# Kernel tuning notes

Measured on AMD Instinct MI355X. Metric: run time of the kernel, lower is better.

## Reference

```python
import jax, jax.numpy as jnp
import numpy as np

MODES = 12

def _conv3x3_circular(x, w, b):
    # x: [B,C,H,W], w: [O,I,3,3] -> circular padding of 1 then VALID conv
    xp = jnp.pad(x, ((0, 0), (0, 0), (1, 1), (1, 1)), mode='wrap')
    y = jax.lax.conv_general_dilated(xp, w, window_strides=(1, 1), padding='VALID',
                                     dimension_numbers=('NCHW', 'OIHW', 'NCHW'))
    return y + b[None, :, None, None]

def _spectral_conv(x, w1, w2):
    # x: [B,C,H,W] real; w1, w2: [C,O,m1,m2] complex
    B, C, H, W = x.shape
    x_ft = jnp.fft.rfft2(x)  # [B,C,H,W//2+1] complex
    m1 = min(MODES, H // 2)
    m2 = min(MODES, W // 2 + 1)
    top = jnp.einsum('bixy,ioxy->boxy', x_ft[:, :, :m1, :m2], w1[:, :, :m1, :m2])
    bot = jnp.einsum('bixy,ioxy->boxy', x_ft[:, :, -m1:, :m2], w2[:, :, :m1, :m2])
    out_ft = jnp.zeros((B, w1.shape[1], H, W // 2 + 1), dtype=x_ft.dtype)
    out_ft = out_ft.at[:, :, :m1, :m2].set(top).at[:, :, -m1:, :m2].set(bot)
    return jnp.fft.irfft2(out_ft, s=(H, W))

def setup_inputs() -> dict:
    key = jax.random.key(0)
    ks = jax.random.split(key, 16)
    width = 32
    scale = 1.0 / (width * width)
    return {
        'x': jax.random.normal(ks[0], (64, 2, 128, 128), dtype=jnp.float32),
        'p_w': jax.random.normal(ks[1], (width, 2, 3, 3), dtype=jnp.float32) * 0.2,
        'p_b': jax.random.normal(ks[2], (width,), dtype=jnp.float32) * 0.1,
        'scw1r': jax.random.uniform(ks[3], (4, width, width, MODES, MODES), dtype=jnp.float32) * scale,
        'scw1i': jax.random.uniform(ks[4], (4, width, width, MODES, MODES), dtype=jnp.float32) * scale,
        'scw2r': jax.random.uniform(ks[5], (4, width, width, MODES, MODES), dtype=jnp.float32) * scale,
        'scw2i': jax.random.uniform(ks[6], (4, width, width, MODES, MODES), dtype=jnp.float32) * scale,
        'ww': jax.random.normal(ks[7], (4, width, width), dtype=jnp.float32) * (1.0 / np.sqrt(width)),
        'wb': jax.random.normal(ks[8], (4, width), dtype=jnp.float32) * 0.1,
        'q1_w': jax.random.normal(ks[9], (128, width), dtype=jnp.float32) * (1.0 / np.sqrt(width)),
        'q1_b': jax.random.normal(ks[10], (128,), dtype=jnp.float32) * 0.1,
        'q2_w': jax.random.normal(ks[11], (1, 128), dtype=jnp.float32) * (1.0 / np.sqrt(128.0)),
        'q2_b': jax.random.normal(ks[12], (1,), dtype=jnp.float32) * 0.1,
    }

def reference(x, p_w, p_b, scw1r, scw1i, scw2r, scw2i, ww, wb, q1_w, q1_b, q2_w, q2_b):
    h = _conv3x3_circular(x, p_w, p_b)  # lifting: [B,2,H,W] -> [B,width,H,W]
    for i in range(4):
        w1 = scw1r[i] + 1j * scw1i[i]
        w2 = scw2r[i] + 1j * scw2i[i]
        x1 = _spectral_conv(h, w1, w2)
        x2 = jnp.einsum('bihw,oi->bohw', h, ww[i]) + wb[i][None, :, None, None]
        h = jax.nn.gelu(x1 + x2, approximate=False)
    g = h.mean(axis=(2, 3))  # [B,width]
    g = jax.nn.gelu(g @ q1_w.T + q1_b, approximate=False)
    g = g @ q2_w.T + q2_b
    return jax.nn.sigmoid(g)
```

## Files before the change

### kernel.cpp

```cpp
#include <hip/hip_runtime.h>
#include <math.h>

#define B 64
#define CIN 2
#define CH 32
#define H 128
#define W 128
#define MODES 12
#define KY 24
#define KX 12
#define HW (H*W)
#define NMODE (KY*KX)

typedef float f32x2 __attribute__((ext_vector_type(2)));
__device__ __forceinline__ f32x2 mk2(float a, float b) { f32x2 r; r.x = a; r.y = b; return r; }

__device__ __forceinline__ float gelu_f(float x) {
    float ax = fabsf(x) * 0.70710678118654752f;
    float t  = __builtin_amdgcn_rcpf(1.0f + 0.3275911f * ax);
    float p  = t * (0.254829592f + t * (-0.284496736f + t * (1.421413741f +
               t * (-1.453152027f + t * 1.061405429f))));
    float e  = __expf(-ax * ax);
    float er = copysignf(1.0f - p * e, x);
    return 0.5f * x * (1.0f + er);
}

__global__ __launch_bounds__(256) void k_init_tables(
        float* cnsWkw, float* cnsH2, float* mnsH2) {
    int t = blockIdx.x * 256 + threadIdx.x;
    const float TWO_PI_OVER = 6.283185307179586476925f / 128.0f;
    if (t < MODES * W) {
        int k = t / W, w = t % W;
        int m = (k * w) & 127;
        float s, c;
        sincosf(TWO_PI_OVER * (float)m, &s, &c);
        cnsWkw[(k * W + w) * 2]     = c;
        cnsWkw[(k * W + w) * 2 + 1] = -s;
    } else if (t < MODES * W + KY * H) {
        int u = t - MODES * W;
        int kyI = u / H, hh = u % H;
        int ky = (kyI < MODES) ? kyI : (H - MODES + (kyI - MODES));
        int m = (ky * hh) & 127;
        float s, c;
        sincosf(TWO_PI_OVER * (float)m, &s, &c);
        cnsH2[(hh * KY + kyI) * 2]     = c;
        cnsH2[(hh * KY + kyI) * 2 + 1] = s;
        mnsH2[(hh * KY + kyI) * 2]     = -s;
        mnsH2[(hh * KY + kyI) * 2 + 1] = c;
    }
}

__global__ __launch_bounds__(256) void k_reorder_w(
        const float* __restrict__ w1r, const float* __restrict__ w1i,
        const float* __restrict__ w2r, const float* __restrict__ w2i,
        float* __restrict__ wR) {
    int idx = blockIdx.x * 256 + threadIdx.x;
    if (idx >= 4 * NMODE * CH * CH) return;
    int o = idx & 31;
    int i = (idx >> 5) & 31;
    int m = (idx >> 10) % NMODE;
    int layer = idx / (NMODE * CH * CH);
    int kyI = m / KX, kx = m % KX;
    const float *sr, *si;
    int row;
    if (kyI < MODES) { sr = w1r; si = w1i; row = kyI; }
    else             { sr = w2r; si = w2i; row = kyI - MODES; }
    int src = ((layer * CH + i) * CH + o) * (MODES * MODES) + row * MODES + kx;
    wR[(size_t)idx * 2]     = sr[src];
    wR[(size_t)idx * 2 + 1] = si[src];
}

__global__ __launch_bounds__(256) void k_transpose_ww(
        const float* __restrict__ ww, float* __restrict__ wwT) {
    int idx = blockIdx.x * 256 + threadIdx.x;
    if (idx >= 4 * CH * CH) return;
    int l = idx / (CH * CH);
    int r = idx % (CH * CH);
    int i = r / CH, o = r % CH;
    wwT[idx] = ww[l * CH * CH + o * CH + i];
}

__global__ __launch_bounds__(128) void k_lift(
        const float* __restrict__ x, const float* __restrict__ pw,
        const float* __restrict__ pb, float* __restrict__ h) {
    int bh = blockIdx.x;
    int b = bh >> 7, hr = bh & 127;
    int w = threadIdx.x;
    int wl = (w + W - 1) & (W - 1), wr2 = (w + 1) & (W - 1);
    float xv[CIN][3][3];
    #pragma unroll
    for (int ic = 0; ic < CIN; ++ic) {
        const float* xc = x + (size_t)(b * CIN + ic) * HW;
        #pragma unroll
        for (int r = 0; r < 3; ++r) {
            int hh = (hr + r - 1 + H) & (H - 1);
            const float* xr = xc + hh * W;
            xv[ic][r][0] = xr[wl];
            xv[ic][r][1] = xr[w];
            xv[ic][r][2] = xr[wr2];
        }
    }
    for (int o = 0; o < CH; ++o) {
        float acc = pb[o];
        const float* wo = pw + o * CIN * 9;
        #pragma unroll
        for (int ic = 0; ic < CIN; ++ic)
            #pragma unroll
            for (int r = 0; r < 3; ++r)
                #pragma unroll
                for (int c3 = 0; c3 < 3; ++c3)
                    acc += xv[ic][r][c3] * wo[ic * 9 + r * 3 + c3];
        h[(size_t)(b * CH + o) * HW + hr * W + w] = acc;
    }
}

__global__ __launch_bounds__(256) void k_dft_w(
        const float* __restrict__ h, const float* __restrict__ cnsWkw,
        float* __restrict__ Xw) {
    __shared__ float xs[64 * 129];
    int row0 = blockIdx.x * 64;
    int tid = threadIdx.x;
    const float4* src = (const float4*)(h + (size_t)row0 * W);
    #pragma unroll
    for (int it = 0; it < 8; ++it) {
        int idx = it * 256 + tid;
        int r = idx >> 5, c4 = idx & 31;
        float4 v = src[idx];
        float* d = xs + r * 129 + c4 * 4;
        d[0] = v.x; d[1] = v.y; d[2] = v.z; d[3] = v.w;
    }
    __syncthreads();
    int r = tid & 63;
    int kp = __builtin_amdgcn_readfirstlane(tid >> 6);
    const f32x2* tw = (const f32x2*)cnsWkw + kp * 3 * W;
    f32x2 a0 = mk2(0.f, 0.f), a1 = mk2(0.f, 0.f), a2 = mk2(0.f, 0.f);
    const float* xr = xs + r * 129;
    #pragma unroll 4
    for (int w = 0; w < W; ++w) {
        float xv = xr[w];
        f32x2 x2 = mk2(xv, xv);
        a0 += x2 * tw[w];
        a1 += x2 * tw[W + w];
        a2 += x2 * tw[2 * W + w];
    }
    float2* dst = (float2*)(Xw + (size_t)(row0 + r) * MODES * 2) + kp * 3;
    dst[0] = make_float2(a0.x, a0.y);
    dst[1] = make_float2(a1.x, a1.y);
    dst[2] = make_float2(a2.x, a2.y);
}

__global__ __launch_bounds__(320) void k_dft_h(
        const float* __restrict__ Xw, const float* __restrict__ cnsH2,
        float* __restrict__ Xf) {
    __shared__ float4 xs4[H * KX / 2];
    const float2* xs = (const float2*)xs4;
    int bc = blockIdx.x;
    int tid = threadIdx.x;
    const float4* src = (const float4*)(Xw + (size_t)bc * H * KX * 2);
    #pragma unroll
    for (int r = 0; r < 3; ++r) {
        int idx = r * 320 + tid;
        if (idx < H * KX / 2) xs4[idx] = src[idx];
    }
    __syncthreads();
    if (tid < KY * KX) {
        int ky = tid / KX, kx = tid % KX;
        const float2* cs = (const float2*)cnsH2 + ky;
        float ar = 0.f, ai = 0.f;
        #pragma unroll 4
        for (int hh = 0; hh < H; ++hh) {
            float2 v = xs[hh * KX + kx];
            float2 t = cs[hh * KY];
            ar += v.x * t.x + v.y * t.y;
            ai += v.y * t.x - v.x * t.y;
        }
        ((float2*)Xf)[(size_t)tid * (B * CH) + bc] = make_float2(ar, ai);
    }
}

__global__ __launch_bounds__(256) void k_specmul(
        const float* __restrict__ Xf, const float* __restrict__ wRl,
        float* __restrict__ Yt) {
    int m = blockIdx.x;
    int o = threadIdx.x & 31;
    int bq = threadIdx.x >> 5;
    const f32x2* X  = (const f32x2*)Xf  + (size_t)m * (B * CH);
    const f32x2* Wm = (const f32x2*)wRl + (size_t)m * (CH * CH);
    f32x2 acc2[8];
    #pragma unroll
    for (int j = 0; j < 8; ++j) acc2[j] = mk2(0.f, 0.f);
    for (int i = 0; i < CH; ++i) {
        f32x2 wv  = Wm[i * CH + o];
        f32x2 wvB = mk2(-wv.y, wv.x);
        #pragma unroll
        for (int j = 0; j < 8; ++j) {
            f32x2 xv = X[(bq * 8 + j) * CH + i];
            acc2[j] += mk2(xv.x, xv.x) * wv + mk2(xv.y, xv.y) * wvB;
        }
    }
    float2* Yp = (float2*)Yt;
    #pragma unroll
    for (int j = 0; j < 8; ++j)
        Yp[((size_t)(bq * 8 + j) * NMODE + m) * CH + o] = make_float2(acc2[j].x, acc2[j].y);
}

__global__ __launch_bounds__(384) void k_idft_h(
        const float* __restrict__ Yt, const float* __restrict__ cnsH2,
        const float* __restrict__ mnsH2, float* __restrict__ Zt) {
    int b = blockIdx.x;
    int hh0 = blockIdx.y * 16;
    int o = threadIdx.x & 31;
    int kx = threadIdx.x >> 5;
    float yr[KY], yi[KY];
    #pragma unroll
    for (int ky = 0; ky < KY; ++ky) {
        float2 v = ((const float2*)Yt)[((size_t)b * NMODE + ky * KX + kx) * CH + o];
        yr[ky] = v.x;  yi[ky] = v.y;
    }
    float sc = (kx == 0 ? 1.0f : 2.0f) / (float)HW;
    #pragma unroll 2
    for (int hr = 0; hr < 16; ++hr) {
        int hh = hh0 + hr;
        const f32x2* cs = (const f32x2*)(cnsH2 + hh * KY * 2);
        const f32x2* ms = (const f32x2*)(mnsH2 + hh * KY * 2);
        f32x2 a = mk2(0.f, 0.f);
        #pragma unroll
        for (int ky = 0; ky < KY; ++ky)
            a += mk2(yr[ky], yr[ky]) * cs[ky] + mk2(yi[ky], yi[ky]) * ms[ky];
        size_t base = ((size_t)(b * H + hh) * 2) * (KX * CH) + kx * CH + o;
        Zt[base]            = a.x * sc;
        Zt[base + KX * CH]  = a.y * sc;
    }
}

template <int LAST>
__global__ __launch_bounds__(512, 4) void k_fused(
        float* __restrict__ h, const float* __restrict__ Zt,
        const float* __restrict__ wwT, const float* __restrict__ wb,
        const float* __restrict__ cnsWkw,
        float* __restrict__ part) {
    __shared__ float hs[CH * W];
    __shared__ float red[8][8];
    int bh = blockIdx.x;
    int b = bh >> 7, hr = bh & 127;
    int tid = threadIdx.x;
    int w = tid & 127;
    int og = __builtin_amdgcn_readfirstlane(tid >> 7);
    const float* hrow = h + (size_t)b * CH * HW + hr * W;
    #pragma unroll
    for (int r = 0; r < 2; ++r) {
        int f4 = r * 512 + tid;
        int i = f4 >> 5;
        int col = (f4 & 31) * 4;
        float4 v = *(const float4*)(hrow + (size_t)i * HW + col);
        *(float4*)(hs + i * W + col) = v;
    }
    float ck[MODES], nsk[MODES];
    const f32x2* cns = (const f32x2*)cnsWkw;
    #pragma unroll
    for (int k = 0; k < MODES; ++k) {
        f32x2 p = cns[k * W + w];
        ck[k]  = p.x;
        nsk[k] = p.y;
    }
    float acc[8];
    const float* wbo = wb + og * 8;
    #pragma unroll
    for (int j = 0; j < 8; ++j) acc[j] = wbo[j];
    __syncthreads();
    #pragma unroll 4
    for (int i = 0; i < CH; ++i) {
        float hv = hs[i * W + w];
        const float* wt = wwT + i * CH + og * 8;
        #pragma unroll
        for (int j = 0; j < 8; ++j) acc[j] += hv * wt[j];
    }
    const float* Zb = Zt + ((size_t)bh * 2) * (KX * CH) + og * 8;
    #pragma unroll
    for (int k = 0; k < MODES; ++k) {
        const float* zr = Zb + k * CH;
        const float* zi = zr + KX * CH;
        float ckv = ck[k], nskv = nsk[k];
        #pragma unroll
        for (int j = 0; j < 8; ++j)
            acc[j] += zr[j] * ckv + zi[j] * nskv;
    }
    if (LAST == 0) {
        float* hout = h + (size_t)(b * CH + og * 8) * HW + hr * W + w;
        #pragma unroll
        for (int j = 0; j < 8; ++j)
            hout[(size_t)j * HW] = gelu_f(acc[j]);
    } else {
        float v[8];
        #pragma unroll
        for (int j = 0; j < 8; ++j) v[j] = gelu_f(acc[j]);
        #pragma unroll
        for (int j = 0; j < 8; ++j)
            #pragma unroll
            for (int off = 32; off > 0; off >>= 1)
                v[j] += __shfl_xor(v[j], off, 64);
        int wave = tid >> 6;
        if ((tid & 63) == 0) {
            #pragma unroll
            for (int j = 0; j < 8; ++j) red[wave][j] = v[j];
        }
        __syncthreads();
        if (tid < CH) {
            float p = red[2 * (tid >> 3)][tid & 7] + red[2 * (tid >> 3) + 1][tid & 7];
            part[((size_t)b * CH + tid) * H + hr] = p;
        }
    }
}

__global__ __launch_bounds__(64) void k_reduce(
        const float* __restrict__ part, float* __restrict__ g) {
    int bc = blockIdx.x;
    int t = threadIdx.x;
    float s = part[(size_t)bc * H + t] + part[(size_t)bc * H + 64 + t];
    #pragma unroll
    for (int off = 32; off > 0; off >>= 1) s += __shfl_down(s, off, 64);
    if (t == 0) g[bc] = s * (1.0f / (float)HW);
}

__global__ __launch_bounds__(128) void k_head(
        const float* __restrict__ g, const float* __restrict__ q1w,
        const float* __restrict__ q1b, const float* __restrict__ q2w,
        const float* __restrict__ q2b, float* __restrict__ out) {
    __shared__ float gs[CH];
    __shared__ float red2[2];
    int b = blockIdx.x;
    int t = threadIdx.x;
    if (t < CH) gs[t] = g[b * CH + t];
    __syncthreads();
    float a = q1b[t];
    #pragma unroll
    for (int c = 0; c < CH; ++c) a += gs[c] * q1w[t * CH + c];
    a = gelu_f(a);
    float hsum = a * q2w[t];
    #pragma unroll
    for (int off = 32; off > 0; off >>= 1) hsum += __shfl_down(hsum, off, 64);
    if ((t & 63) == 0) red2[t >> 6] = hsum;
    __syncthreads();
    if (t == 0) {
        float logit = red2[0] + red2[1] + q2b[0];
        out[b] = 1.0f / (1.0f + expf(-logit));
    }
}

extern "C" void kernel_launch(void* const* d_in, const int* in_sizes, int n_in,
                              void* d_out, int out_size, void* d_ws, size_t ws_size,
                              hipStream_t stream) {
    const float* x   = (const float*)d_in[0];
    const float* p_w = (const float*)d_in[1];
    const float* p_b = (const float*)d_in[2];
    const float* w1r = (const float*)d_in[3];
    const float* w1i = (const float*)d_in[4];
    const float* w2r = (const float*)d_in[5];
    const float* w2i = (const float*)d_in[6];
    const float* ww  = (const float*)d_in[7];
    const float* wb  = (const float*)d_in[8];
    const float* q1w = (const float*)d_in[9];
    const float* q1b = (const float*)d_in[10];
    const float* q2w = (const float*)d_in[11];
    const float* q2b = (const float*)d_in[12];
    float* out = (float*)d_out;

    float* ws = (float*)d_ws;
    size_t off = 0;
    auto alloc = [&](size_t n) {
        float* p = ws + off;
        off += (n + 63) & ~(size_t)63;
        return p;
    };
    float* cnsWkw = alloc(MODES * W * 2);
    float* cnsH2  = alloc(H * KY * 2);
    float* mnsH2  = alloc(H * KY * 2);
    float* hBuf = alloc((size_t)B * CH * HW);
    float* XwZ  = alloc((size_t)B * CH * H * KX * 2);
    float* Xf   = alloc((size_t)NMODE * B * CH * 2);
    float* Yt   = alloc((size_t)B * NMODE * CH * 2);
    float* wR   = alloc((size_t)4 * NMODE * CH * CH * 2);
    float* wwT  = alloc(4 * CH * CH);
    float* part = alloc((size_t)B * CH * H);
    float* g    = alloc(B * CH);

    k_init_tables<<<(MODES * W + KY * H + 255) / 256, 256, 0, stream>>>(
        cnsWkw, cnsH2, mnsH2);
    k_reorder_w<<<(4 * NMODE * CH * CH + 255) / 256, 256, 0, stream>>>(
        w1r, w1i, w2r, w2i, wR);
    k_transpose_ww<<<(4 * CH * CH + 255) / 256, 256, 0, stream>>>(ww, wwT);

    k_lift<<<B * H, 128, 0, stream>>>(x, p_w, p_b, hBuf);

    for (int layer = 0; layer < 4; ++layer) {
        k_dft_w<<<(B * CH * H) / 64, 256, 0, stream>>>(hBuf, cnsWkw, XwZ);
        k_dft_h<<<B * CH, 320, 0, stream>>>(XwZ, cnsH2, Xf);
        k_specmul<<<NMODE, 256, 0, stream>>>(
            Xf, wR + (size_t)layer * NMODE * CH * CH * 2, Yt);
        k_idft_h<<<dim3(B, 8), 384, 0, stream>>>(Yt, cnsH2, mnsH2, XwZ);
        if (layer < 3)
            k_fused<0><<<B * H, 512, 0, stream>>>(
                hBuf, XwZ, wwT + layer * CH * CH, wb + layer * CH, cnsWkw, part);
        else
            k_fused<1><<<B * H, 512, 0, stream>>>(
                hBuf, XwZ, wwT + layer * CH * CH, wb + layer * CH, cnsWkw, part);
    }

    k_reduce<<<B * CH, 64, 0, stream>>>(part, g);
    k_head<<<B, 128, 0, stream>>>(g, q1w, q1b, q2w, q2b, out);
}
```

Measured before the change: 818.9 us.

## Fuse W-direction DFT into lift and fused-layer epilogues

Removes the standalone k_dft_w kernel by computing the width-direction truncated DFT inside k_lift and at the end of k_fused<0>, using the freshly produced row still held in shared memory. This drops one launch per layer and the re-read of the full h tensor from global memory. The cost is extra shared memory (about 16.5KB per block on top of the existing 16KB), an extra __syncthreads, and a tail phase in which only 128 of 512 threads work, which may lower occupancy and add latency to those kernels. Xw and Zt now get separate buffers, since the fused kernel reads Zt while it writes Xw.

```diff
diff --git a/kernel.cpp b/kernel.cpp
--- a/kernel.cpp
+++ b/kernel.cpp
@@ -80,12 +80,41 @@
     wwT[idx] = ww[l * CH * CH + o * CH + i];
 }
 
-__global__ __launch_bounds__(128) void k_lift(
+__device__ __forceinline__ void dft_tail(
+        const float* xs2, const float* __restrict__ cnsWkw,
+        float* __restrict__ Xw, int b, int hr, int tid) {
+    if (tid < 128) {
+        int c = tid & 31;
+        int kp = tid >> 5;
+        const f32x2* tw = (const f32x2*)cnsWkw + kp * 3 * W;
+        f32x2 a0 = mk2(0.f, 0.f), a1 = mk2(0.f, 0.f), a2 = mk2(0.f, 0.f);
+        const float* xr = xs2 + c * 129;
+        #pragma unroll 4
+        for (int w = 0; w < W; ++w) {
+            float xv = xr[w];
+            f32x2 x2 = mk2(xv, xv);
+            a0 += x2 * tw[w];
+            a1 += x2 * tw[W + w];
+            a2 += x2 * tw[2 * W + w];
+        }
+        int row = (b * CH + c) * H + hr;
+        float2* dst = (float2*)(Xw + (size_t)row * MODES * 2) + kp * 3;
+        dst[0] = make_float2(a0.x, a0.y);
+        dst[1] = make_float2(a1.x, a1.y);
+        dst[2] = make_float2(a2.x, a2.y);
+    }
+}
+
+__global__ __launch_bounds__(512) void k_lift(
         const float* __restrict__ x, const float* __restrict__ pw,
-        const float* __restrict__ pb, float* __restrict__ h) {
+        const float* __restrict__ pb, float* __restrict__ h,
+        const float* __restrict__ cnsWkw, float* __restrict__ Xw) {
+    __shared__ float xs2[CH * 129];
     int bh = blockIdx.x;
     int b = bh >> 7, hr = bh & 127;
-    int w = threadIdx.x;
+    int tid = threadIdx.x;
+    int w = tid & 127;
+    int og = __builtin_amdgcn_readfirstlane(tid >> 7);
     int wl = (w + W - 1) & (W - 1), wr2 = (w + 1) & (W - 1);
     float xv[CIN][3][3];
     #pragma unroll
@@ -100,7 +129,9 @@
             xv[ic][r][2] = xr[wr2];
         }
     }
-    for (int o = 0; o < CH; ++o) {
+    #pragma unroll
+    for (int j = 0; j < 8; ++j) {
+        int o = og * 8 + j;
         float acc = pb[o];
         const float* wo = pw + o * CIN * 9;
         #pragma unroll
@@ -111,42 +142,10 @@
                 for (int c3 = 0; c3 < 3; ++c3)
                     acc += xv[ic][r][c3] * wo[ic * 9 + r * 3 + c3];
         h[(size_t)(b * CH + o) * HW + hr * W + w] = acc;
-    }
-}
-
-__global__ __launch_bounds__(256) void k_dft_w(
-        const float* __restrict__ h, const float* __restrict__ cnsWkw,
-        float* __restrict__ Xw) {
-    __shared__ float xs[64 * 129];
-    int row0 = blockIdx.x * 64;
-    int tid = threadIdx.x;
-    const float4* src = (const float4*)(h + (size_t)row0 * W);
-    #pragma unroll
-    for (int it = 0; it < 8; ++it) {
-        int idx = it * 256 + tid;
-        int r = idx >> 5, c4 = idx & 31;
-        float4 v = src[idx];
-        float* d = xs + r * 129 + c4 * 4;
-        d[0] = v.x; d[1] = v.y; d[2] = v.z; d[3] = v.w;
+        xs2[o * 129 + w] = acc;
     }
     __syncthreads();
-    int r = tid & 63;
-    int kp = __builtin_amdgcn_readfirstlane(tid >> 6);
-    const f32x2* tw = (const f32x2*)cnsWkw + kp * 3 * W;
-    f32x2 a0 = mk2(0.f, 0.f), a1 = mk2(0.f, 0.f), a2 = mk2(0.f, 0.f);
-    const float* xr = xs + r * 129;
-    #pragma unroll 4
-    for (int w = 0; w < W; ++w) {
-        float xv = xr[w];
-        f32x2 x2 = mk2(xv, xv);
-        a0 += x2 * tw[w];
-        a1 += x2 * tw[W + w];
-        a2 += x2 * tw[2 * W + w];
-    }
-    float2* dst = (float2*)(Xw + (size_t)(row0 + r) * MODES * 2) + kp * 3;
-    dst[0] = make_float2(a0.x, a0.y);
-    dst[1] = make_float2(a1.x, a1.y);
-    dst[2] = make_float2(a2.x, a2.y);
+    dft_tail(xs2, cnsWkw, Xw, b, hr, tid);
 }
 
 __global__ __launch_bounds__(320) void k_dft_h(
@@ -238,8 +237,9 @@
         float* __restrict__ h, const float* __restrict__ Zt,
         const float* __restrict__ wwT, const float* __restrict__ wb,
         const float* __restrict__ cnsWkw,
-        float* __restrict__ part) {
+        float* __restrict__ part, float* __restrict__ Xw) {
     __shared__ float hs[CH * W];
+    __shared__ float xbuf[LAST ? 64 : CH * 129];
     __shared__ float red[8][8];
     int bh = blockIdx.x;
     int b = bh >> 7, hr = bh & 127;
@@ -288,8 +288,13 @@
     if (LAST == 0) {
         float* hout = h + (size_t)(b * CH + og * 8) * HW + hr * W + w;
         #pragma unroll
-        for (int j = 0; j < 8; ++j)
-            hout[(size_t)j * HW] = gelu_f(acc[j]);
+        for (int j = 0; j < 8; ++j) {
+            float gv = gelu_f(acc[j]);
+            hout[(size_t)j * HW] = gv;
+            xbuf[(og * 8 + j) * 129 + w] = gv;
+        }
+        __syncthreads();
+        dft_tail(xbuf, cnsWkw, Xw, b, hr, tid);
     } else {
         float v[8];
         #pragma unroll
@@ -376,7 +381,8 @@
     float* cnsH2  = alloc(H * KY * 2);
     float* mnsH2  = alloc(H * KY * 2);
     float* hBuf = alloc((size_t)B * CH * HW);
-    float* XwZ  = alloc((size_t)B * CH * H * KX * 2);
+    float* Xw   = alloc((size_t)B * CH * H * KX * 2);
+    float* Zt   = alloc((size_t)B * CH * H * KX * 2);
     float* Xf   = alloc((size_t)NMODE * B * CH * 2);
     float* Yt   = alloc((size_t)B * NMODE * CH * 2);
     float* wR   = alloc((size_t)4 * NMODE * CH * CH * 2);
@@ -390,20 +396,19 @@
         w1r, w1i, w2r, w2i, wR);
     k_transpose_ww<<<(4 * CH * CH + 255) / 256, 256, 0, stream>>>(ww, wwT);
 
-    k_lift<<<B * H, 128, 0, stream>>>(x, p_w, p_b, hBuf);
+    k_lift<<<B * H, 512, 0, stream>>>(x, p_w, p_b, hBuf, cnsWkw, Xw);
 
     for (int layer = 0; layer < 4; ++layer) {
-        k_dft_w<<<(B * CH * H) / 64, 256, 0, stream>>>(hBuf, cnsWkw, XwZ);
-        k_dft_h<<<B * CH, 320, 0, stream>>>(XwZ, cnsH2, Xf);
+        k_dft_h<<<B * CH, 320, 0, stream>>>(Xw, cnsH2, Xf);
         k_specmul<<<NMODE, 256, 0, stream>>>(
             Xf, wR + (size_t)layer * NMODE * CH * CH * 2, Yt);
-        k_idft_h<<<dim3(B, 8), 384, 0, stream>>>(Yt, cnsH2, mnsH2, XwZ);
+        k_idft_h<<<dim3(B, 8), 384, 0, stream>>>(Yt, cnsH2, mnsH2, Zt);
         if (layer < 3)
             k_fused<0><<<B * H, 512, 0, stream>>>(
-                hBuf, XwZ, wwT + layer * CH * CH, wb + layer * CH, cnsWkw, part);
+                hBuf, Zt, wwT + layer * CH * CH, wb + layer * CH, cnsWkw, part, Xw);
         else
             k_fused<1><<<B * H, 512, 0, stream>>>(
-                hBuf, XwZ, wwT + layer * CH * CH, wb + layer * CH, cnsWkw, part);
+                hBuf, Zt, wwT + layer * CH * CH, wb + layer * CH, cnsWkw, part, Xw);
     }
 
     k_reduce<<<B * CH, 64, 0, stream>>>(part, g);
```

Result: slower. 954.0 us (+16.5%).
